# Optimization experiments

Measured on AMD Instinct MI355X. Metric: run time of the kernel, lower is better.

Reference implementation:

```python
import jax, jax.numpy as jnp
import numpy as np

TOP_K = 48
NUM_RBF = 16
NUM_RBF_SC = 8
MAXREL = 32
EDGE_F = 128
EPS_D = 1e-6
LN_EPS = 1e-5


def gather_nodes(nodes, idx):
    # nodes: [B, L, C], idx: [B, L, K] -> [B, L, K, C]
    return jax.vmap(lambda n, i: n[i])(nodes, idx)


def rbf(D, count):
    # D: [..., ] -> [..., count]; mu in [2, 22], sigma = 20/count
    mu = jnp.linspace(2.0, 22.0, count)
    sigma = (22.0 - 2.0) / count
    return jnp.exp(-(((D[..., None] - mu) / sigma) ** 2))


def layer_norm(x, g, b):
    mu = jnp.mean(x, -1, keepdims=True)
    var = jnp.mean((x - mu) ** 2, -1, keepdims=True)
    return g * (x - mu) / jnp.sqrt(var + LN_EPS) + b


def setup_inputs() -> dict:
    key = jax.random.key(0)
    ks = jax.random.split(key, 8)
    B, Lr = 1, 1024
    X = jax.random.normal(ks[0], (B, Lr, 37, 3), dtype=jnp.float32)
    mask = jnp.ones((B, Lr), dtype=jnp.float32)
    atom_mask = jnp.ones((B, Lr, 37), dtype=jnp.float32)
    residue_idx = jnp.arange(B * Lr, dtype=jnp.int64 if jax.config.jax_enable_x64 else jnp.int32).reshape(B, Lr)
    dihedral_mask = jnp.ones((B, Lr), dtype=jnp.float32)
    chain_labels = jnp.zeros((B, Lr), dtype=jnp.int32)
    W_pos = jax.random.normal(ks[1], (16, 2 * MAXREL + 2), dtype=jnp.float32) * 0.1
    b_pos = jnp.zeros((16,), dtype=jnp.float32)
    W_e = jax.random.normal(ks[2], (EDGE_F, 16 + NUM_RBF * 25), dtype=jnp.float32) * 0.05
    g_e = jnp.ones((EDGE_F,), dtype=jnp.float32)
    be_e = jnp.zeros((EDGE_F,), dtype=jnp.float32)
    W_s = jax.random.normal(ks[3], (EDGE_F, NUM_RBF_SC * 32 * 5), dtype=jnp.float32) * 0.05
    g_s = jnp.ones((EDGE_F,), dtype=jnp.float32)
    b_s = jnp.zeros((EDGE_F,), dtype=jnp.float32)
    return {"X": X, "L": 1024, "mask": mask, "atom_mask": atom_mask,
            "residue_idx": residue_idx, "dihedral_mask": dihedral_mask,
            "chain_labels": chain_labels, "W_pos": W_pos, "b_pos": b_pos,
            "W_e": W_e, "g_e": g_e, "be_e": be_e, "W_s": W_s, "g_s": g_s, "b_s": b_s}


def reference(X, L, mask, atom_mask, residue_idx, dihedral_mask, chain_labels,
              W_pos, b_pos, W_e, g_e, be_e, W_s, g_s, b_s):
    # Virtual Cb from ideal geometry
    b_v = X[:, :, 1, :] - X[:, :, 0, :]
    c_v = X[:, :, 2, :] - X[:, :, 1, :]
    a_v = jnp.cross(b_v, c_v)
    Cb = -0.58273431 * a_v + 0.56802827 * b_v - 0.54067466 * c_v + X[:, :, 1, :]
    Ca = X[:, :, 1, :]
    N = X[:, :, 0, :]
    C = X[:, :, 2, :]
    O = X[:, :, 4, :]

    # _dist: masked pairwise Ca distances + top-k smallest
    mask2d = mask[:, None, :] * mask[:, :, None]  # [B, L, L]
    dX = Ca[:, :, None, :] - Ca[:, None, :, :]
    D = mask2d * jnp.sqrt(jnp.sum(dX ** 2, -1) + EPS_D)
    D_max = jnp.max(D, -1, keepdims=True)
    D_adj = D + (1.0 - mask2d) * D_max
    neg_vals, E_idx = jax.lax.top_k(-D_adj, TOP_K)
    D_neighbors = -neg_vals  # [B, L, K]

    coords = {'N': N, 'Ca': Ca, 'C': C, 'O': O, 'Cb': Cb}
    pairs = [('N','N'),('C','C'),('O','O'),('Cb','Cb'),('Ca','N'),('Ca','C'),('Ca','O'),
             ('Ca','Cb'),('N','C'),('N','O'),('N','Cb'),('Cb','C'),('Cb','O'),('O','C'),
             ('N','Ca'),('C','Ca'),('O','Ca'),('Cb','Ca'),('C','N'),('O','N'),('Cb','N'),
             ('C','Cb'),('O','Cb'),('C','O')]
    A_st = jnp.stack([coords[a] for a, _ in pairs])  # [24, B, L, 3]
    B_st = jnp.stack([coords[b] for _, b in pairs])
    B_nb = jax.vmap(gather_nodes, (0, None))(B_st, E_idx)  # [24, B, L, K, 3]
    Dp = jnp.sqrt(jnp.sum((A_st[:, :, :, None, :] - B_nb) ** 2, -1) + EPS_D)  # [24,B,L,K]
    RBF_pairs = rbf(Dp, NUM_RBF)  # [24, B, L, K, 16]
    Bt, Lr, K = E_idx.shape
    RBF_pairs = jnp.moveaxis(RBF_pairs, 0, 3).reshape(Bt, Lr, K, 24 * NUM_RBF)
    RBF_all = jnp.concatenate([rbf(D_neighbors, NUM_RBF), RBF_pairs], -1)  # [B,L,K,400]

    # Positional encodings
    ri_nb = gather_nodes(residue_idx[..., None], E_idx)[..., 0]  # [B,L,K]
    offset = residue_idx[:, :, None] - ri_nb
    ch_nb = gather_nodes(chain_labels[..., None], E_idx)[..., 0]
    E_chains = (chain_labels[:, :, None] - ch_nb == 0).astype(jnp.int32)
    d = jnp.clip(offset + MAXREL, 0, 2 * MAXREL) * E_chains + (1 - E_chains) * (2 * MAXREL + 1)
    d_onehot = jax.nn.one_hot(d, 2 * MAXREL + 2, dtype=jnp.float32)
    E_positional = d_onehot @ W_pos.T + b_pos
    E = jnp.concatenate([E_positional, RBF_all], -1)  # [B,L,K,416]

    # Sidechain RBFs on the first min(100, K) neighbors
    Ks = min(100, K)
    E_idx_sub = E_idx[:, :, :Ks]
    am_g = gather_nodes(atom_mask, E_idx_sub)  # [B,L,Ks,37]
    S = X[:, :, 5:37, :]  # [B,L,32,3]
    S_nb = gather_nodes(S.reshape(Bt, Lr, 32 * 3), E_idx_sub).reshape(Bt, Lr, Ks, 32, 3)
    anchors = jnp.stack([N, Ca, C, O, Cb], 2)  # [B,L,5,3], anchor order matches loop order
    Ds = jnp.sqrt(jnp.sum((anchors[:, :, None, :, None, :] - S_nb[:, :, :, None, :, :]) ** 2, -1) + EPS_D)
    # Ds: [B,L,Ks,5,32]; rbf_side -> [B,L,Ks,5,32,8]; masked by neighbor atom mask
    RBF_s = rbf(Ds, NUM_RBF_SC) * am_g[:, :, :, None, 5:37, None]
    E_s = RBF_s.reshape(Bt, Lr, Ks, 5 * 32 * NUM_RBF_SC)  # [B,L,Ks,1280]

    E_s = layer_norm(E_s @ W_s.T, g_s, b_s)
    E = layer_norm(E @ W_e.T, g_e, be_e)
    return (E, E_idx, E_s, E_idx_sub)
```

## Files before the change

### kernel.cpp

```cpp
#include <hip/hip_runtime.h>
#include <math.h>

#define LRES 1024
#define TOPK 48
#define NEDGE (LRES*TOPK)

typedef short short8 __attribute__((ext_vector_type(8)));
typedef float f32x4  __attribute__((ext_vector_type(4)));

#define OUT_E     0
#define OUT_EIDX  6291456
#define OUT_ES    6340608
#define OUT_EIDX2 12632064

#define WS_COORDS 0
#define WS_DNB    15360
#define WS_EIDX   64512
#define WS_WPE    113664
#define WS_WPS    140288

#define DE 1.06666667f
#define QE 0.10273976f
#define DS 1.14285714f
#define QS 0.07337053f

__constant__ int PA[24] = {0,2,3,4,1,1,1,1,0,0,0,4,4,3,0,2,3,4,2,3,4,2,3,2};
__constant__ int PB[24] = {0,2,3,4,0,2,3,4,2,3,4,2,3,2,1,1,1,1,0,0,0,4,4,3};

__device__ inline short f2bf(float f) {
    unsigned u = __float_as_uint(f);
    unsigned r = (u + 0x7FFFu + ((u >> 16) & 1u)) >> 16;
    return (short)r;
}

__device__ inline short8 pack8(const float* fv) {
    union { short8 s; unsigned u[4]; } r;
    #pragma unroll
    for (int i = 0; i < 4; ++i)
        r.u[i] = __builtin_amdgcn_perm(__float_as_uint(fv[2*i+1]),
                                       __float_as_uint(fv[2*i]), 0x07060302u);
    return r.s;
}

__global__ void k_prep(const float* __restrict__ X, const float* __restrict__ We,
                       const float* __restrict__ Ws, float* __restrict__ coords,
                       short* __restrict__ WpE, short* __restrict__ WpS) {
    if (blockIdx.x < 640) {
        int t = blockIdx.x * 256 + threadIdx.x;
        if (t < 8*13*64*8) {
            int j = t & 7, lane = (t >> 3) & 63, g = t >> 9;
            int ks = g % 13, nt = g / 13;
            int n = nt*16 + (lane & 15), k = ks*32 + (lane >> 4)*8 + j;
            WpE[t] = f2bf(We[n*416 + k]);
        }
        if (t < 8*40*64*8) {
            int j = t & 7, lane = (t >> 3) & 63, g = t >> 9;
            int ks = g % 40, nt = g / 40;
            int n = nt*16 + (lane & 15), k = ks*32 + (lane >> 4)*8 + j;
            WpS[t] = f2bf(Ws[n*1280 + k]);
        }
    } else {
        int r = (blockIdx.x - 640) * 256 + threadIdx.x;
        if (r >= LRES) return;
        const float* xr = X + r * 37 * 3;
        float N[3], Ca[3], C[3], O[3], bv[3], cv[3], av[3];
        #pragma unroll
        for (int d = 0; d < 3; ++d) {
            N[d]  = xr[0*3 + d];  Ca[d] = xr[1*3 + d];
            C[d]  = xr[2*3 + d];  O[d]  = xr[4*3 + d];
            bv[d] = Ca[d] - N[d]; cv[d] = C[d] - Ca[d];
        }
        av[0] = bv[1]*cv[2] - bv[2]*cv[1];
        av[1] = bv[2]*cv[0] - bv[0]*cv[2];
        av[2] = bv[0]*cv[1] - bv[1]*cv[0];
        float* o = coords + r * 15;
        #pragma unroll
        for (int d = 0; d < 3; ++d) {
            float Cb = -0.58273431f*av[d] + 0.56802827f*bv[d] - 0.54067466f*cv[d] + Ca[d];
            o[0*3+d] = N[d]; o[1*3+d] = Ca[d]; o[2*3+d] = C[d];
            o[3*3+d] = O[d]; o[4*3+d] = Cb;
        }
    }
}

__global__ __launch_bounds__(256) void k_topk(const float* __restrict__ X,
                                              const float* __restrict__ mask,
                                              float* __restrict__ Dnb,
                                              int* __restrict__ Eidx,
                                              float* __restrict__ out) {
    __shared__ float sCa[LRES*3];
    __shared__ float sM[LRES];
    int t = threadIdx.x;
    for (int j = t; j < LRES; j += 256) {
        sCa[j*3+0] = X[j*111 + 3];
        sCa[j*3+1] = X[j*111 + 4];
        sCa[j*3+2] = X[j*111 + 5];
        sM[j] = mask[j];
    }
    __syncthreads();
    int w = t >> 6, lane = t & 63;
    int i = blockIdx.x * 4 + w;
    float cx = sCa[i*3], cy = sCa[i*3+1], cz = sCa[i*3+2];
    float mi = sM[i];
    float dv[16], m2v[16];
    float lmax = -1e30f;
    #pragma unroll
    for (int s = 0; s < 16; ++s) {
        int j = s*64 + lane;
        float dx = cx - sCa[j*3], dy = cy - sCa[j*3+1], dz = cz - sCa[j*3+2];
        float d  = sqrtf(dx*dx + dy*dy + dz*dz + 1e-6f);
        float m2 = mi * sM[j];
        dv[s] = m2 * d; m2v[s] = m2;
        lmax = fmaxf(lmax, dv[s]);
    }
    #pragma unroll
    for (int off = 32; off; off >>= 1) lmax = fmaxf(lmax, __shfl_xor(lmax, off));
    unsigned long long key[16];
    unsigned long long mkey = ~0ull; int mslot = 0;
    #pragma unroll
    for (int s = 0; s < 16; ++s) {
        float dadj = dv[s] + (1.0f - m2v[s]) * lmax;
        key[s] = (((unsigned long long)__float_as_uint(dadj)) << 10) | (unsigned)(s*64 + lane);
        if (key[s] < mkey) { mkey = key[s]; mslot = s; }
    }
    for (int it = 0; it < TOPK; ++it) {
        unsigned long long wk = mkey;
        #pragma unroll
        for (int off = 32; off; off >>= 1) {
            unsigned long long o = __shfl_xor(wk, off);
            wk = (o < wk) ? o : wk;
        }
        if (lane == 0) {
            int j = (int)(wk & 1023u);
            int id = i*TOPK + it;
            Dnb[id]  = __uint_as_float((unsigned)(wk >> 10));
            Eidx[id] = j;
            out[OUT_EIDX  + id] = (float)j;
            out[OUT_EIDX2 + id] = (float)j;
        }
        if (mkey == wk) {
            key[mslot] = ~0ull;
            mkey = ~0ull;
            #pragma unroll
            for (int s = 0; s < 16; ++s)
                if (key[s] < mkey) { mkey = key[s]; mslot = s; }
        }
    }
}

__global__ __launch_bounds__(256, 3) void k_edgeE(const float* __restrict__ coords,
                                                  const short* __restrict__ WpE,
                                                  const float* __restrict__ Dnb,
                                                  const int* __restrict__ Eidx,
                                                  const int* __restrict__ ri,
                                                  const int* __restrict__ ch,
                                                  const float* __restrict__ Wpos,
                                                  const float* __restrict__ bpos,
                                                  const float* __restrict__ ge,
                                                  const float* __restrict__ be,
                                                  float* __restrict__ out) {
    __shared__ float sA[32*15], sB[32*15];
    __shared__ float u_hbuf[32*132];
    __shared__ int   sdpos[32];
    __shared__ float part[32*8], part2[32*8], smu[32], srs[32];
    float* sdist = u_hbuf;
    float* sposf = u_hbuf + 32*27;
    int t = threadIdx.x;
    int id0 = blockIdx.x * 32;

    if (t < 32) {
        int id = id0 + t, i = id / TOPK, j = Eidx[id];
        int off = ri[i] - ri[j];
        sdpos[t] = (ch[i] == ch[j]) ? min(max(off + 32, 0), 64) : 65;
        sdist[t*27] = Dnb[id];
    }
    for (int it = t; it < 32*15; it += 256) {
        int e = it / 15, q = it % 15;
        int id = id0 + e, i = id / TOPK, j = Eidx[id];
        sA[e*15+q] = coords[i*15+q];
        sB[e*15+q] = coords[j*15+q];
    }
    __syncthreads();
    for (int it = t; it < 32*24; it += 256) {
        int e = it / 24, p = it % 24, a = PA[p], b = PB[p];
        float dx = sA[e*15+a*3+0] - sB[e*15+b*3+0];
        float dy = sA[e*15+a*3+1] - sB[e*15+b*3+1];
        float dz = sA[e*15+a*3+2] - sB[e*15+b*3+2];
        sdist[e*27 + 1 + p] = sqrtf(dx*dx + dy*dy + dz*dz + 1e-6f);
    }
    for (int it = t; it < 32*16; it += 256) {
        int e = it >> 4, c = it & 15;
        sposf[e*17 + c] = Wpos[c*66 + sdpos[e]] + bpos[c];
    }
    __syncthreads();

    int w = t >> 6, lane = t & 63, quad = lane >> 4, l16 = lane & 15;
    f32x4 acc[2][8] = {};
    const short8* bp = (const short8*)WpE;
    float rb = (quad & 1) ? 8.0f*DE : 0.0f;

    for (int ks = w; ks < 13; ks += 4) {
        short8 afrag[2];
        #pragma unroll
        for (int mt = 0; mt < 2; ++mt) {
            int e = mt*16 + l16;
            float fv[8];
            if (ks == 0 && quad < 2) {
                #pragma unroll
                for (int j = 0; j < 8; ++j) fv[j] = sposf[e*17 + quad*8 + j];
            } else {
                int p = (ks == 0) ? 0 : (2*ks - 1 + (quad >> 1));
                float d = sdist[e*27 + p];
                float u = fmaf(d, 0.8f, -1.6f) - rb;
                float e0 = __expf(-u*u);
                float g  = __expf(DE*(u + u - DE));
                fv[0] = e0;
                #pragma unroll
                for (int r = 1; r < 8; ++r) { e0 *= g; g *= QE; fv[r] = e0; }
            }
            afrag[mt] = pack8(fv);
        }
        #pragma unroll
        for (int nt = 0; nt < 8; ++nt) {
            short8 b = bp[(nt*13 + ks)*64 + lane];
            acc[0][nt] = __builtin_amdgcn_mfma_f32_16x16x32_bf16(afrag[0], b, acc[0][nt], 0,0,0);
            acc[1][nt] = __builtin_amdgcn_mfma_f32_16x16x32_bf16(afrag[1], b, acc[1][nt], 0,0,0);
        }
    }

    float* hbuf = u_hbuf;
    __syncthreads();
    for (int ww = 0; ww < 4; ++ww) {
        if (w == ww) {
            #pragma unroll
            for (int mt = 0; mt < 2; ++mt)
            #pragma unroll
            for (int nt = 0; nt < 8; ++nt)
            #pragma unroll
            for (int r = 0; r < 4; ++r) {
                int e = mt*16 + quad*4 + r;
                float* p = &hbuf[e*132 + nt*16 + l16];
                if (ww == 0) *p = acc[mt][nt][r]; else *p += acc[mt][nt][r];
            }
        }
        __syncthreads();
    }
    {
        int e = t >> 3, p = t & 7;
        float s = 0.f, s2 = 0.f;
        #pragma unroll
        for (int q = 0; q < 16; ++q) {
            float x = hbuf[e*132 + p*16 + q];
            s += x; s2 += x*x;
        }
        part[e*8+p] = s; part2[e*8+p] = s2;
    }
    __syncthreads();
    if (t < 32) {
        float s = 0.f, s2 = 0.f;
        #pragma unroll
        for (int p = 0; p < 8; ++p) { s += part[t*8+p]; s2 += part2[t*8+p]; }
        float mu = s * (1.0f/128.0f);
        float var = s2 * (1.0f/128.0f) - mu*mu;
        smu[t] = mu; srs[t] = rsqrtf(var + 1e-5f);
    }
    __syncthreads();
    for (int it = t; it < 32*128; it += 256) {
        int e = it >> 7, f = it & 127;
        float x = hbuf[e*132 + f];
        out[OUT_E + (size_t)(id0 + e)*128 + f] = ge[f] * (x - smu[e]) * srs[e] + be[f];
    }
}

__global__ __launch_bounds__(256, 3) void k_edgeS(const float* __restrict__ coords,
                                                  const float* __restrict__ X,
                                                  const float* __restrict__ amask,
                                                  const short* __restrict__ WpS,
                                                  const int* __restrict__ Eidx,
                                                  const float* __restrict__ gs,
                                                  const float* __restrict__ bs,
                                                  float* __restrict__ out) {
    __shared__ float sA[32*15];
    __shared__ float u_hbuf[32*132];
    __shared__ float sam[32*35];
    __shared__ int   sj[32];
    __shared__ float part[32*8], part2[32*8], smu[32], srs[32];
    float* sS = u_hbuf;
    int t = threadIdx.x;
    int id0 = blockIdx.x * 32;

    if (t < 32) sj[t] = Eidx[id0 + t];
    __syncthreads();
    for (int it = t; it < 32*15; it += 256) {
        int e = it / 15, q = it % 15;
        sA[e*15+q] = coords[((id0 + e) / TOPK)*15 + q];
    }
    for (int it = t; it < 32*96; it += 256) {
        int e = it / 96, q = it % 96;
        sS[e*100 + q] = X[(sj[e]*37 + 5)*3 + q];
    }
    for (int it = t; it < 32*32; it += 256) {
        int e = it >> 5, s = it & 31;
        sam[e*35 + s] = amask[sj[e]*37 + 5 + s];
    }
    __syncthreads();

    int w = t >> 6, lane = t & 63, quad = lane >> 4, l16 = lane & 15;
    f32x4 acc[2][8] = {};
    const short8* bp = (const short8*)WpS;

    for (int ks = w; ks < 40; ks += 4) {
        int ach = ks >> 3, s = (ks & 7)*4 + quad;
        short8 afrag[2];
        #pragma unroll
        for (int mt = 0; mt < 2; ++mt) {
            int e = mt*16 + l16;
            float dx = sA[e*15 + ach*3 + 0] - sS[e*100 + s*3 + 0];
            float dy = sA[e*15 + ach*3 + 1] - sS[e*100 + s*3 + 1];
            float dz = sA[e*15 + ach*3 + 2] - sS[e*100 + s*3 + 2];
            float d  = sqrtf(dx*dx + dy*dy + dz*dz + 1e-6f);
            float u  = fmaf(d, 0.4f, -0.8f);
            float e0 = __expf(-u*u) * sam[e*35 + s];
            float g  = __expf(DS*(u + u - DS));
            float fv[8];
            fv[0] = e0;
            #pragma unroll
            for (int r = 1; r < 8; ++r) { e0 *= g; g *= QS; fv[r] = e0; }
            afrag[mt] = pack8(fv);
        }
        #pragma unroll
        for (int nt = 0; nt < 8; ++nt) {
            short8 b = bp[(nt*40 + ks)*64 + lane];
            acc[0][nt] = __builtin_amdgcn_mfma_f32_16x16x32_bf16(afrag[0], b, acc[0][nt], 0,0,0);
            acc[1][nt] = __builtin_amdgcn_mfma_f32_16x16x32_bf16(afrag[1], b, acc[1][nt], 0,0,0);
        }
    }

    float* hbuf = u_hbuf;
    __syncthreads();
    for (int ww = 0; ww < 4; ++ww) {
        if (w == ww) {
            #pragma unroll
            for (int mt = 0; mt < 2; ++mt)
            #pragma unroll
            for (int nt = 0; nt < 8; ++nt)
            #pragma unroll
            for (int r = 0; r < 4; ++r) {
                int e = mt*16 + quad*4 + r;
                float* p = &hbuf[e*132 + nt*16 + l16];
                if (ww == 0) *p = acc[mt][nt][r]; else *p += acc[mt][nt][r];
            }
        }
        __syncthreads();
    }
    {
        int e = t >> 3, p = t & 7;
        float s = 0.f, s2 = 0.f;
        #pragma unroll
        for (int q = 0; q < 16; ++q) {
            float x = hbuf[e*132 + p*16 + q];
            s += x; s2 += x*x;
        }
        part[e*8+p] = s; part2[e*8+p] = s2;
    }
    __syncthreads();
    if (t < 32) {
        float s = 0.f, s2 = 0.f;
        #pragma unroll
        for (int p = 0; p < 8; ++p) { s += part[t*8+p]; s2 += part2[t*8+p]; }
        float mu = s * (1.0f/128.0f);
        float var = s2 * (1.0f/128.0f) - mu*mu;
        smu[t] = mu; srs[t] = rsqrtf(var + 1e-5f);
    }
    __syncthreads();
    for (int it = t; it < 32*128; it += 256) {
        int e = it >> 7, f = it & 127;
        float x = hbuf[e*132 + f];
        out[OUT_ES + (size_t)(id0 + e)*128 + f] = gs[f] * (x - smu[e]) * srs[e] + bs[f];
    }
}

extern "C" void kernel_launch(void* const* d_in, const int* in_sizes, int n_in,
                              void* d_out, int out_size, void* d_ws, size_t ws_size,
                              hipStream_t stream) {
    (void)in_sizes; (void)n_in; (void)out_size; (void)ws_size;
    const float* X     = (const float*)d_in[0];
    const float* mask  = (const float*)d_in[2];
    const float* amask = (const float*)d_in[3];
    const int*   ri    = (const int*)d_in[4];
    const int*   ch    = (const int*)d_in[6];
    const float* Wpos  = (const float*)d_in[7];
    const float* bpos  = (const float*)d_in[8];
    const float* We    = (const float*)d_in[9];
    const float* ge    = (const float*)d_in[10];
    const float* be    = (const float*)d_in[11];
    const float* Ws    = (const float*)d_in[12];
    const float* gs    = (const float*)d_in[13];
    const float* bs    = (const float*)d_in[14];

    float* out    = (float*)d_out;
    float* ws     = (float*)d_ws;
    float* coords = ws + WS_COORDS;
    float* Dnb    = ws + WS_DNB;
    int*   Eidx   = (int*)(ws + WS_EIDX);
    short* WpE    = (short*)(ws + WS_WPE);
    short* WpS    = (short*)(ws + WS_WPS);

    k_prep <<<dim3(644),  dim3(256), 0, stream>>>(X, We, Ws, coords, WpE, WpS);
    k_topk <<<dim3(256),  dim3(256), 0, stream>>>(X, mask, Dnb, Eidx, out);
    k_edgeE<<<dim3(1536), dim3(256), 0, stream>>>(coords, WpE, Dnb, Eidx, ri, ch,
                                                  Wpos, bpos, ge, be, out);
    k_edgeS<<<dim3(1536), dim3(256), 0, stream>>>(coords, X, amask, WpS, Eidx,
                                                  gs, bs, out);
}
```

Before: 200.3 us.

## Merge prep/topk and edgeE/edgeS kernels into two launches with register-held sidechain gathers

```diff
diff --git a/kernel.cpp b/kernel.cpp
--- a/kernel.cpp
+++ b/kernel.cpp
@@ -42,27 +42,93 @@
     return r.s;
 }
 
-__global__ void k_prep(const float* __restrict__ X, const float* __restrict__ We,
-                       const float* __restrict__ Ws, float* __restrict__ coords,
-                       short* __restrict__ WpE, short* __restrict__ WpS) {
-    if (blockIdx.x < 640) {
-        int t = blockIdx.x * 256 + threadIdx.x;
-        if (t < 8*13*64*8) {
-            int j = t & 7, lane = (t >> 3) & 63, g = t >> 9;
-            int ks = g % 13, nt = g / 13;
+__global__ __launch_bounds__(256) void k_pre(const float* __restrict__ X,
+                                             const float* __restrict__ mask,
+                                             const float* __restrict__ We,
+                                             const float* __restrict__ Ws,
+                                             float* __restrict__ coords,
+                                             short* __restrict__ WpE,
+                                             short* __restrict__ WpS,
+                                             float* __restrict__ Dnb,
+                                             int* __restrict__ Eidx,
+                                             float* __restrict__ out) {
+    int blk = blockIdx.x, t = threadIdx.x;
+    if (blk < 256) {
+        __shared__ float sCa[LRES*3];
+        __shared__ float sM[LRES];
+        for (int j = t; j < LRES; j += 256) {
+            sCa[j*3+0] = X[j*111 + 3];
+            sCa[j*3+1] = X[j*111 + 4];
+            sCa[j*3+2] = X[j*111 + 5];
+            sM[j] = mask[j];
+        }
+        __syncthreads();
+        int w = t >> 6, lane = t & 63;
+        int i = blk * 4 + w;
+        float cx = sCa[i*3], cy = sCa[i*3+1], cz = sCa[i*3+2];
+        float mi = sM[i];
+        float dv[16], m2v[16];
+        float lmax = -1e30f;
+        #pragma unroll
+        for (int s = 0; s < 16; ++s) {
+            int j = s*64 + lane;
+            float dx = cx - sCa[j*3], dy = cy - sCa[j*3+1], dz = cz - sCa[j*3+2];
+            float d  = __builtin_amdgcn_sqrtf(dx*dx + dy*dy + dz*dz + 1e-6f);
+            float m2 = mi * sM[j];
+            dv[s] = m2 * d; m2v[s] = m2;
+            lmax = fmaxf(lmax, dv[s]);
+        }
+        #pragma unroll
+        for (int off = 32; off; off >>= 1) lmax = fmaxf(lmax, __shfl_xor(lmax, off));
+        unsigned long long key[16];
+        unsigned long long mkey = ~0ull; int mslot = 0;
+        #pragma unroll
+        for (int s = 0; s < 16; ++s) {
+            float dadj = dv[s] + (1.0f - m2v[s]) * lmax;
+            key[s] = (((unsigned long long)__float_as_uint(dadj)) << 10) | (unsigned)(s*64 + lane);
+            if (key[s] < mkey) { mkey = key[s]; mslot = s; }
+        }
+        for (int it = 0; it < TOPK; ++it) {
+            unsigned long long wk = mkey;
+            #pragma unroll
+            for (int off = 32; off; off >>= 1) {
+                unsigned long long o = __shfl_xor(wk, off);
+                wk = (o < wk) ? o : wk;
+            }
+            if (lane == 0) {
+                int j = (int)(wk & 1023u);
+                int id = i*TOPK + it;
+                Dnb[id]  = __uint_as_float((unsigned)(wk >> 10));
+                Eidx[id] = j;
+                out[OUT_EIDX  + id] = (float)j;
+                out[OUT_EIDX2 + id] = (float)j;
+            }
+            if (mkey == wk) {
+                key[mslot] = ~0ull;
+                mkey = ~0ull;
+                #pragma unroll
+                for (int s = 0; s < 16; ++s)
+                    if (key[s] < mkey) { mkey = key[s]; mslot = s; }
+            }
+        }
+    } else if (blk < 896) {
+        int g = (blk - 256) * 256 + t;
+        if (g < 8*13*64*8) {
+            int j = g & 7, lane = (g >> 3) & 63, gg = g >> 9;
+            int ks = gg % 13, nt = gg / 13;
             int n = nt*16 + (lane & 15), k = ks*32 + (lane >> 4)*8 + j;
-            WpE[t] = f2bf(We[n*416 + k]);
-        }
-        if (t < 8*40*64*8) {
-            int j = t & 7, lane = (t >> 3) & 63, g = t >> 9;
-            int ks = g % 40, nt = g / 40;
+            WpE[g] = f2bf(We[n*416 + k]);
+        }
+        if (g < 8*40*64*8) {
+            int j = g & 7, lane = (g >> 3) & 63, gg = g >> 9;
+            int ks = gg % 40, nt = gg / 40;
             int n = nt*16 + (lane & 15), k = ks*32 + (lane >> 4)*8 + j;
-            WpS[t] = f2bf(Ws[n*1280 + k]);
+            WpS[g] = f2bf(Ws[n*1280 + k]);
         }
     } else {
-        int r = (blockIdx.x - 640) * 256 + threadIdx.x;
+        int r = (blk - 896) * 256 + t;
         if (r >= LRES) return;
-        const float* xr = X + r * 37 * 3;
+        const float* xr = X + r * 111;
         float N[3], Ca[3], C[3], O[3], bv[3], cv[3], av[3];
         #pragma unroll
         for (int d = 0; d < 3; ++d) {
@@ -83,300 +149,258 @@
     }
 }
 
-__global__ __launch_bounds__(256) void k_topk(const float* __restrict__ X,
-                                              const float* __restrict__ mask,
-                                              float* __restrict__ Dnb,
-                                              int* __restrict__ Eidx,
-                                              float* __restrict__ out) {
-    __shared__ float sCa[LRES*3];
-    __shared__ float sM[LRES];
+__global__ __launch_bounds__(256, 2) void k_edge(const float* __restrict__ coords,
+                                                 const float* __restrict__ X,
+                                                 const float* __restrict__ amask,
+                                                 const short* __restrict__ WpE,
+                                                 const short* __restrict__ WpS,
+                                                 const float* __restrict__ Dnb,
+                                                 const int* __restrict__ Eidx,
+                                                 const int* __restrict__ ri,
+                                                 const int* __restrict__ ch,
+                                                 const float* __restrict__ Wpos,
+                                                 const float* __restrict__ bpos,
+                                                 const float* __restrict__ ge,
+                                                 const float* __restrict__ be,
+                                                 const float* __restrict__ gs,
+                                                 const float* __restrict__ bs,
+                                                 float* __restrict__ out) {
+    __shared__ float smem[5808];
     int t = threadIdx.x;
-    for (int j = t; j < LRES; j += 256) {
-        sCa[j*3+0] = X[j*111 + 3];
-        sCa[j*3+1] = X[j*111 + 4];
-        sCa[j*3+2] = X[j*111 + 5];
-        sM[j] = mask[j];
-    }
-    __syncthreads();
-    int w = t >> 6, lane = t & 63;
-    int i = blockIdx.x * 4 + w;
-    float cx = sCa[i*3], cy = sCa[i*3+1], cz = sCa[i*3+2];
-    float mi = sM[i];
-    float dv[16], m2v[16];
-    float lmax = -1e30f;
-    #pragma unroll
-    for (int s = 0; s < 16; ++s) {
-        int j = s*64 + lane;
-        float dx = cx - sCa[j*3], dy = cy - sCa[j*3+1], dz = cz - sCa[j*3+2];
-        float d  = sqrtf(dx*dx + dy*dy + dz*dz + 1e-6f);
-        float m2 = mi * sM[j];
-        dv[s] = m2 * d; m2v[s] = m2;
-        lmax = fmaxf(lmax, dv[s]);
-    }
-    #pragma unroll
-    for (int off = 32; off; off >>= 1) lmax = fmaxf(lmax, __shfl_xor(lmax, off));
-    unsigned long long key[16];
-    unsigned long long mkey = ~0ull; int mslot = 0;
-    #pragma unroll
-    for (int s = 0; s < 16; ++s) {
-        float dadj = dv[s] + (1.0f - m2v[s]) * lmax;
-        key[s] = (((unsigned long long)__float_as_uint(dadj)) << 10) | (unsigned)(s*64 + lane);
-        if (key[s] < mkey) { mkey = key[s]; mslot = s; }
-    }
-    for (int it = 0; it < TOPK; ++it) {
-        unsigned long long wk = mkey;
-        #pragma unroll
-        for (int off = 32; off; off >>= 1) {
-            unsigned long long o = __shfl_xor(wk, off);
-            wk = (o < wk) ? o : wk;
-        }
-        if (lane == 0) {
-            int j = (int)(wk & 1023u);
-            int id = i*TOPK + it;
-            Dnb[id]  = __uint_as_float((unsigned)(wk >> 10));
-            Eidx[id] = j;
-            out[OUT_EIDX  + id] = (float)j;
-            out[OUT_EIDX2 + id] = (float)j;
-        }
-        if (mkey == wk) {
-            key[mslot] = ~0ull;
-            mkey = ~0ull;
-            #pragma unroll
-            for (int s = 0; s < 16; ++s)
-                if (key[s] < mkey) { mkey = key[s]; mslot = s; }
-        }
-    }
-}
-
-__global__ __launch_bounds__(256, 3) void k_edgeE(const float* __restrict__ coords,
-                                                  const short* __restrict__ WpE,
-                                                  const float* __restrict__ Dnb,
-                                                  const int* __restrict__ Eidx,
-                                                  const int* __restrict__ ri,
-                                                  const int* __restrict__ ch,
-                                                  const float* __restrict__ Wpos,
-                                                  const float* __restrict__ bpos,
-                                                  const float* __restrict__ ge,
-                                                  const float* __restrict__ be,
-                                                  float* __restrict__ out) {
-    __shared__ float sA[32*15], sB[32*15];
-    __shared__ float u_hbuf[32*132];
-    __shared__ int   sdpos[32];
-    __shared__ float part[32*8], part2[32*8], smu[32], srs[32];
-    float* sdist = u_hbuf;
-    float* sposf = u_hbuf + 32*27;
-    int t = threadIdx.x;
-    int id0 = blockIdx.x * 32;
-
-    if (t < 32) {
-        int id = id0 + t, i = id / TOPK, j = Eidx[id];
-        int off = ri[i] - ri[j];
-        sdpos[t] = (ch[i] == ch[j]) ? min(max(off + 32, 0), 64) : 65;
-        sdist[t*27] = Dnb[id];
-    }
-    for (int it = t; it < 32*15; it += 256) {
-        int e = it / 15, q = it % 15;
-        int id = id0 + e, i = id / TOPK, j = Eidx[id];
-        sA[e*15+q] = coords[i*15+q];
-        sB[e*15+q] = coords[j*15+q];
-    }
-    __syncthreads();
-    for (int it = t; it < 32*24; it += 256) {
-        int e = it / 24, p = it % 24, a = PA[p], b = PB[p];
-        float dx = sA[e*15+a*3+0] - sB[e*15+b*3+0];
-        float dy = sA[e*15+a*3+1] - sB[e*15+b*3+1];
-        float dz = sA[e*15+a*3+2] - sB[e*15+b*3+2];
-        sdist[e*27 + 1 + p] = sqrtf(dx*dx + dy*dy + dz*dz + 1e-6f);
-    }
-    for (int it = t; it < 32*16; it += 256) {
-        int e = it >> 4, c = it & 15;
-        sposf[e*17 + c] = Wpos[c*66 + sdpos[e]] + bpos[c];
-    }
-    __syncthreads();
-
     int w = t >> 6, lane = t & 63, quad = lane >> 4, l16 = lane & 15;
-    f32x4 acc[2][8] = {};
-    const short8* bp = (const short8*)WpE;
-    float rb = (quad & 1) ? 8.0f*DE : 0.0f;
-
-    for (int ks = w; ks < 13; ks += 4) {
-        short8 afrag[2];
+
+    if (blockIdx.x < 1536) {
+        float* u_hbuf = smem;
+        float* sA3    = smem + 4224;
+        float* part   = smem + 4272;
+        float* part2  = smem + 4528;
+        float* smu    = smem + 4784;
+        float* srs    = smem + 4816;
+        int id0 = blockIdx.x * 32;
+        int i0 = id0 / TOPK;
+
+        if (t < 45) {
+            int rr = i0 + t / 15;
+            if (rr > LRES-1) rr = LRES-1;
+            sA3[t] = coords[rr*15 + t%15];
+        }
+        int s1 = 4*w + quad;
+        float S[2][2][3], am[2][2];
+        int im[2];
         #pragma unroll
         for (int mt = 0; mt < 2; ++mt) {
-            int e = mt*16 + l16;
-            float fv[8];
-            if (ks == 0 && quad < 2) {
-                #pragma unroll
-                for (int j = 0; j < 8; ++j) fv[j] = sposf[e*17 + quad*8 + j];
-            } else {
-                int p = (ks == 0) ? 0 : (2*ks - 1 + (quad >> 1));
-                float d = sdist[e*27 + p];
-                float u = fmaf(d, 0.8f, -1.6f) - rb;
-                float e0 = __expf(-u*u);
-                float g  = __expf(DE*(u + u - DE));
-                fv[0] = e0;
-                #pragma unroll
-                for (int r = 1; r < 8; ++r) { e0 *= g; g *= QE; fv[r] = e0; }
-            }
-            afrag[mt] = pack8(fv);
-        }
-        #pragma unroll
-        for (int nt = 0; nt < 8; ++nt) {
-            short8 b = bp[(nt*13 + ks)*64 + lane];
-            acc[0][nt] = __builtin_amdgcn_mfma_f32_16x16x32_bf16(afrag[0], b, acc[0][nt], 0,0,0);
-            acc[1][nt] = __builtin_amdgcn_mfma_f32_16x16x32_bf16(afrag[1], b, acc[1][nt], 0,0,0);
-        }
-    }
-
-    float* hbuf = u_hbuf;
-    __syncthreads();
-    for (int ww = 0; ww < 4; ++ww) {
-        if (w == ww) {
-            #pragma unroll
-            for (int mt = 0; mt < 2; ++mt)
-            #pragma unroll
-            for (int nt = 0; nt < 8; ++nt)
-            #pragma unroll
-            for (int r = 0; r < 4; ++r) {
-                int e = mt*16 + quad*4 + r;
-                float* p = &hbuf[e*132 + nt*16 + l16];
-                if (ww == 0) *p = acc[mt][nt][r]; else *p += acc[mt][nt][r];
-            }
-        }
-        __syncthreads();
-    }
-    {
-        int e = t >> 3, p = t & 7;
-        float s = 0.f, s2 = 0.f;
-        #pragma unroll
-        for (int q = 0; q < 16; ++q) {
-            float x = hbuf[e*132 + p*16 + q];
-            s += x; s2 += x*x;
-        }
-        part[e*8+p] = s; part2[e*8+p] = s2;
-    }
-    __syncthreads();
-    if (t < 32) {
-        float s = 0.f, s2 = 0.f;
-        #pragma unroll
-        for (int p = 0; p < 8; ++p) { s += part[t*8+p]; s2 += part2[t*8+p]; }
-        float mu = s * (1.0f/128.0f);
-        float var = s2 * (1.0f/128.0f) - mu*mu;
-        smu[t] = mu; srs[t] = rsqrtf(var + 1e-5f);
-    }
-    __syncthreads();
-    for (int it = t; it < 32*128; it += 256) {
-        int e = it >> 7, f = it & 127;
-        float x = hbuf[e*132 + f];
-        out[OUT_E + (size_t)(id0 + e)*128 + f] = ge[f] * (x - smu[e]) * srs[e] + be[f];
-    }
-}
-
-__global__ __launch_bounds__(256, 3) void k_edgeS(const float* __restrict__ coords,
-                                                  const float* __restrict__ X,
-                                                  const float* __restrict__ amask,
-                                                  const short* __restrict__ WpS,
-                                                  const int* __restrict__ Eidx,
-                                                  const float* __restrict__ gs,
-                                                  const float* __restrict__ bs,
-                                                  float* __restrict__ out) {
-    __shared__ float sA[32*15];
-    __shared__ float u_hbuf[32*132];
-    __shared__ float sam[32*35];
-    __shared__ int   sj[32];
-    __shared__ float part[32*8], part2[32*8], smu[32], srs[32];
-    float* sS = u_hbuf;
-    int t = threadIdx.x;
-    int id0 = blockIdx.x * 32;
-
-    if (t < 32) sj[t] = Eidx[id0 + t];
-    __syncthreads();
-    for (int it = t; it < 32*15; it += 256) {
-        int e = it / 15, q = it % 15;
-        sA[e*15+q] = coords[((id0 + e) / TOPK)*15 + q];
-    }
-    for (int it = t; it < 32*96; it += 256) {
-        int e = it / 96, q = it % 96;
-        sS[e*100 + q] = X[(sj[e]*37 + 5)*3 + q];
-    }
-    for (int it = t; it < 32*32; it += 256) {
-        int e = it >> 5, s = it & 31;
-        sam[e*35 + s] = amask[sj[e]*37 + 5 + s];
-    }
-    __syncthreads();
-
-    int w = t >> 6, lane = t & 63, quad = lane >> 4, l16 = lane & 15;
-    f32x4 acc[2][8] = {};
-    const short8* bp = (const short8*)WpS;
-
-    for (int ks = w; ks < 40; ks += 4) {
-        int ach = ks >> 3, s = (ks & 7)*4 + quad;
-        short8 afrag[2];
-        #pragma unroll
-        for (int mt = 0; mt < 2; ++mt) {
-            int e = mt*16 + l16;
-            float dx = sA[e*15 + ach*3 + 0] - sS[e*100 + s*3 + 0];
-            float dy = sA[e*15 + ach*3 + 1] - sS[e*100 + s*3 + 1];
-            float dz = sA[e*15 + ach*3 + 2] - sS[e*100 + s*3 + 2];
-            float d  = sqrtf(dx*dx + dy*dy + dz*dz + 1e-6f);
-            float u  = fmaf(d, 0.4f, -0.8f);
-            float e0 = __expf(-u*u) * sam[e*35 + s];
-            float g  = __expf(DS*(u + u - DS));
-            float fv[8];
-            fv[0] = e0;
-            #pragma unroll
-            for (int r = 1; r < 8; ++r) { e0 *= g; g *= QS; fv[r] = e0; }
-            afrag[mt] = pack8(fv);
-        }
-        #pragma unroll
-        for (int nt = 0; nt < 8; ++nt) {
-            short8 b = bp[(nt*40 + ks)*64 + lane];
-            acc[0][nt] = __builtin_amdgcn_mfma_f32_16x16x32_bf16(afrag[0], b, acc[0][nt], 0,0,0);
-            acc[1][nt] = __builtin_amdgcn_mfma_f32_16x16x32_bf16(afrag[1], b, acc[1][nt], 0,0,0);
-        }
-    }
-
-    float* hbuf = u_hbuf;
-    __syncthreads();
-    for (int ww = 0; ww < 4; ++ww) {
-        if (w == ww) {
-            #pragma unroll
-            for (int mt = 0; mt < 2; ++mt)
-            #pragma unroll
-            for (int nt = 0; nt < 8; ++nt)
-            #pragma unroll
-            for (int r = 0; r < 4; ++r) {
-                int e = mt*16 + quad*4 + r;
-                float* p = &hbuf[e*132 + nt*16 + l16];
-                if (ww == 0) *p = acc[mt][nt][r]; else *p += acc[mt][nt][r];
-            }
-        }
-        __syncthreads();
-    }
-    {
-        int e = t >> 3, p = t & 7;
-        float s = 0.f, s2 = 0.f;
-        #pragma unroll
-        for (int q = 0; q < 16; ++q) {
-            float x = hbuf[e*132 + p*16 + q];
-            s += x; s2 += x*x;
-        }
-        part[e*8+p] = s; part2[e*8+p] = s2;
-    }
-    __syncthreads();
-    if (t < 32) {
-        float s = 0.f, s2 = 0.f;
-        #pragma unroll
-        for (int p = 0; p < 8; ++p) { s += part[t*8+p]; s2 += part2[t*8+p]; }
-        float mu = s * (1.0f/128.0f);
-        float var = s2 * (1.0f/128.0f) - mu*mu;
-        smu[t] = mu; srs[t] = rsqrtf(var + 1e-5f);
-    }
-    __syncthreads();
-    for (int it = t; it < 32*128; it += 256) {
-        int e = it >> 7, f = it & 127;
-        float x = hbuf[e*132 + f];
-        out[OUT_ES + (size_t)(id0 + e)*128 + f] = gs[f] * (x - smu[e]) * srs[e] + bs[f];
+            int id = id0 + mt*16 + l16;
+            int j  = Eidx[id];
+            im[mt] = id / TOPK;
+            const float* xp = X + (j*37 + 5)*3;
+            const float* ap = amask + j*37 + 5;
+            #pragma unroll
+            for (int h = 0; h < 2; ++h) {
+                int s = s1 + h*16;
+                S[mt][h][0] = xp[s*3+0];
+                S[mt][h][1] = xp[s*3+1];
+                S[mt][h][2] = xp[s*3+2];
+                am[mt][h]   = ap[s];
+            }
+        }
+        __syncthreads();
+
+        f32x4 acc[2][8] = {};
+        const short8* bp = (const short8*)WpS;
+
+        for (int a = 0; a < 5; ++a) {
+            float A[2][3];
+            #pragma unroll
+            for (int mt = 0; mt < 2; ++mt) {
+                int base = (im[mt] - i0)*15 + a*3;
+                A[mt][0] = sA3[base+0];
+                A[mt][1] = sA3[base+1];
+                A[mt][2] = sA3[base+2];
+            }
+            #pragma unroll
+            for (int h = 0; h < 2; ++h) {
+                int ks = a*8 + w + h*4;
+                short8 afrag[2];
+                #pragma unroll
+                for (int mt = 0; mt < 2; ++mt) {
+                    float dx = A[mt][0] - S[mt][h][0];
+                    float dy = A[mt][1] - S[mt][h][1];
+                    float dz = A[mt][2] - S[mt][h][2];
+                    float d  = __builtin_amdgcn_sqrtf(fmaf(dz,dz,fmaf(dy,dy,fmaf(dx,dx,1e-6f))));
+                    float u  = fmaf(d, 0.4f, -0.8f);
+                    float e0 = __expf(-u*u) * am[mt][h];
+                    float g  = __expf(fmaf(2.0f*DS, u, -DS*DS));
+                    float fv[8];
+                    fv[0] = e0;
+                    #pragma unroll
+                    for (int r = 1; r < 8; ++r) { e0 *= g; g *= QS; fv[r] = e0; }
+                    afrag[mt] = pack8(fv);
+                }
+                #pragma unroll
+                for (int nt = 0; nt < 8; ++nt) {
+                    short8 b = bp[(nt*40 + ks)*64 + lane];
+                    acc[0][nt] = __builtin_amdgcn_mfma_f32_16x16x32_bf16(afrag[0], b, acc[0][nt], 0,0,0);
+                    acc[1][nt] = __builtin_amdgcn_mfma_f32_16x16x32_bf16(afrag[1], b, acc[1][nt], 0,0,0);
+                }
+            }
+        }
+
+        float* hbuf = u_hbuf;
+        __syncthreads();
+        for (int ww = 0; ww < 4; ++ww) {
+            if (w == ww) {
+                #pragma unroll
+                for (int mt = 0; mt < 2; ++mt)
+                #pragma unroll
+                for (int nt = 0; nt < 8; ++nt)
+                #pragma unroll
+                for (int r = 0; r < 4; ++r) {
+                    int e = mt*16 + quad*4 + r;
+                    float* p = &hbuf[e*132 + nt*16 + l16];
+                    if (ww == 0) *p = acc[mt][nt][r]; else *p += acc[mt][nt][r];
+                }
+            }
+            __syncthreads();
+        }
+        {
+            int e = t >> 3, p = t & 7;
+            float s = 0.f, s2 = 0.f;
+            #pragma unroll
+            for (int q = 0; q < 16; ++q) {
+                float x = hbuf[e*132 + p*16 + q];
+                s += x; s2 += x*x;
+            }
+            part[e*8+p] = s; part2[e*8+p] = s2;
+        }
+        __syncthreads();
+        if (t < 32) {
+            float s = 0.f, s2 = 0.f;
+            #pragma unroll
+            for (int p = 0; p < 8; ++p) { s += part[t*8+p]; s2 += part2[t*8+p]; }
+            float mu = s * (1.0f/128.0f);
+            float var = s2 * (1.0f/128.0f) - mu*mu;
+            smu[t] = mu; srs[t] = rsqrtf(var + 1e-5f);
+        }
+        __syncthreads();
+        for (int it = t; it < 32*128; it += 256) {
+            int e = it >> 7, f = it & 127;
+            float x = hbuf[e*132 + f];
+            out[OUT_ES + (size_t)(id0 + e)*128 + f] = gs[f] * (x - smu[e]) * srs[e] + bs[f];
+        }
+    } else {
+        float* sA     = smem;
+        float* sB     = smem + 480;
+        float* u_hbuf = smem + 960;
+        float* part   = smem + 5184;
+        float* part2  = smem + 5440;
+        float* smu    = smem + 5696;
+        float* srs    = smem + 5728;
+        int*   sdpos  = (int*)(smem + 5760);
+        float* sdist  = u_hbuf;
+        float* sposf  = u_hbuf + 32*27;
+        int id0 = (blockIdx.x - 1536) * 32;
+
+        if (t < 32) {
+            int id = id0 + t, i = id / TOPK, j = Eidx[id];
+            int off = ri[i] - ri[j];
+            sdpos[t] = (ch[i] == ch[j]) ? min(max(off + 32, 0), 64) : 65;
+            sdist[t*27] = Dnb[id];
+        }
+        for (int it = t; it < 32*15; it += 256) {
+            int e = it / 15, q = it % 15;
+            int id = id0 + e, i = id / TOPK, j = Eidx[id];
+            sA[e*15+q] = coords[i*15+q];
+            sB[e*15+q] = coords[j*15+q];
+        }
+        __syncthreads();
+        for (int it = t; it < 32*24; it += 256) {
+            int e = it / 24, p = it % 24, a = PA[p], b = PB[p];
+            float dx = sA[e*15+a*3+0] - sB[e*15+b*3+0];
+            float dy = sA[e*15+a*3+1] - sB[e*15+b*3+1];
+            float dz = sA[e*15+a*3+2] - sB[e*15+b*3+2];
+            sdist[e*27 + 1 + p] = __builtin_amdgcn_sqrtf(dx*dx + dy*dy + dz*dz + 1e-6f);
+        }
+        for (int it = t; it < 32*16; it += 256) {
+            int e = it >> 4, c = it & 15;
+            sposf[e*17 + c] = Wpos[c*66 + sdpos[e]] + bpos[c];
+        }
+        __syncthreads();
+
+        f32x4 acc[2][8] = {};
+        const short8* bp = (const short8*)WpE;
+        float rb = (quad & 1) ? 8.0f*DE : 0.0f;
+
+        for (int ks = w; ks < 13; ks += 4) {
+            short8 afrag[2];
+            #pragma unroll
+            for (int mt = 0; mt < 2; ++mt) {
+                int e = mt*16 + l16;
+                float fv[8];
+                if (ks == 0 && quad < 2) {
+                    #pragma unroll
+                    for (int j = 0; j < 8; ++j) fv[j] = sposf[e*17 + quad*8 + j];
+                } else {
+                    int p = (ks == 0) ? 0 : (2*ks - 1 + (quad >> 1));
+                    float d = sdist[e*27 + p];
+                    float u = fmaf(d, 0.8f, -1.6f) - rb;
+                    float e0 = __expf(-u*u);
+                    float g  = __expf(fmaf(2.0f*DE, u, -DE*DE));
+                    fv[0] = e0;
+                    #pragma unroll
+                    for (int r = 1; r < 8; ++r) { e0 *= g; g *= QE; fv[r] = e0; }
+                }
+                afrag[mt] = pack8(fv);
+            }
+            #pragma unroll
+            for (int nt = 0; nt < 8; ++nt) {
+                short8 b = bp[(nt*13 + ks)*64 + lane];
+                acc[0][nt] = __builtin_amdgcn_mfma_f32_16x16x32_bf16(afrag[0], b, acc[0][nt], 0,0,0);
+                acc[1][nt] = __builtin_amdgcn_mfma_f32_16x16x32_bf16(afrag[1], b, acc[1][nt], 0,0,0);
+            }
+        }
+
+        float* hbuf = u_hbuf;
+        __syncthreads();
+        for (int ww = 0; ww < 4; ++ww) {
+            if (w == ww) {
+                #pragma unroll
+                for (int mt = 0; mt < 2; ++mt)
+                #pragma unroll
+                for (int nt = 0; nt < 8; ++nt)
+                #pragma unroll
+                for (int r = 0; r < 4; ++r) {
+                    int e = mt*16 + quad*4 + r;
+                    float* p = &hbuf[e*132 + nt*16 + l16];
+                    if (ww == 0) *p = acc[mt][nt][r]; else *p += acc[mt][nt][r];
+                }
+            }
+            __syncthreads();
+        }
+        {
+            int e = t >> 3, p = t & 7;
+            float s = 0.f, s2 = 0.f;
+            #pragma unroll
+            for (int q = 0; q < 16; ++q) {
+                float x = hbuf[e*132 + p*16 + q];
+                s += x; s2 += x*x;
+            }
+            part[e*8+p] = s; part2[e*8+p] = s2;
+        }
+        __syncthreads();
+        if (t < 32) {
+            float s = 0.f, s2 = 0.f;
+            #pragma unroll
+            for (int p = 0; p < 8; ++p) { s += part[t*8+p]; s2 += part2[t*8+p]; }
+            float mu = s * (1.0f/128.0f);
+            float var = s2 * (1.0f/128.0f) - mu*mu;
+            smu[t] = mu; srs[t] = rsqrtf(var + 1e-5f);
+        }
+        __syncthreads();
+        for (int it = t; it < 32*128; it += 256) {
+            int e = it >> 7, f = it & 127;
+            float x = hbuf[e*132 + f];
+            out[OUT_E + (size_t)(id0 + e)*128 + f] = ge[f] * (x - smu[e]) * srs[e] + be[f];
+        }
     }
 }
 
@@ -406,10 +430,9 @@
     short* WpE    = (short*)(ws + WS_WPE);
     short* WpS    = (short*)(ws + WS_WPS);
 
-    k_prep <<<dim3(644),  dim3(256), 0, stream>>>(X, We, Ws, coords, WpE, WpS);
-    k_topk <<<dim3(256),  dim3(256), 0, stream>>>(X, mask, Dnb, Eidx, out);
-    k_edgeE<<<dim3(1536), dim3(256), 0, stream>>>(coords, WpE, Dnb, Eidx, ri, ch,
-                                                  Wpos, bpos, ge, be, out);
-    k_edgeS<<<dim3(1536), dim3(256), 0, stream>>>(coords, X, amask, WpS, Eidx,
-                                                  gs, bs, out);
+    k_pre <<<dim3(900),  dim3(256), 0, stream>>>(X, mask, We, Ws, coords,
+                                                 WpE, WpS, Dnb, Eidx, out);
+    k_edge<<<dim3(3072), dim3(256), 0, stream>>>(coords, X, amask, WpE, WpS,
+                                                 Dnb, Eidx, ri, ch, Wpos, bpos,
+                                                 ge, be, gs, bs, out);
 }
```

New measurement: 187.6 us. -6.3%, faster.
